# Kernel tuning notes

Measured on AMD Instinct MI355X. Metric: run time of the kernel, lower is better.

## Reference

```python
import jax, jax.numpy as jnp
import numpy as np

B, NA, C, NG = 32, 32768, 81, 24
POS_IOU, NEG_IOU, NPR = 0.5, 0.4, 3
VXY, VWH = 0.1, 0.2
NEG_BIG = 1e30


def cxcywh_to_xyxy(b):
    xy, wh = b[..., :2], b[..., 2:]
    return jnp.concatenate([xy - 0.5 * wh, xy + 0.5 * wh], axis=-1)


def box_iou_xyxy(a, g):
    # a: [Na,4], g: [Ng,4] -> [Na,Ng]
    lt = jnp.maximum(a[:, None, :2], g[None, :, :2])
    rb = jnp.minimum(a[:, None, 2:], g[None, :, 2:])
    wh = jnp.clip(rb - lt, 0.0)
    inter = wh[..., 0] * wh[..., 1]
    area_a = (a[:, 2] - a[:, 0]) * (a[:, 3] - a[:, 1])
    area_g = (g[:, 2] - g[:, 0]) * (g[:, 3] - g[:, 1])
    union = area_a[:, None] + area_g[None, :] - inter
    return inter / jnp.maximum(union, 1e-12)


def encode_ssd(gt, anc):
    # gt, anc: [N,4] cxcywh
    txy = (gt[:, :2] - anc[:, :2]) / anc[:, 2:] / VXY
    twh = jnp.log(gt[:, 2:] / anc[:, 2:]) / VWH
    return jnp.concatenate([txy, twh], axis=-1)


def match_one(anchors, gt_b, gt_l):
    # anchors: [Na,4], gt_b: [Ng,4], gt_l: [Ng]
    iou = box_iou_xyxy(cxcywh_to_xyxy(anchors), cxcywh_to_xyxy(gt_b))  # [Na,Ng]
    iou_max = iou.max(axis=1)
    gt_idx = jnp.argmax(iou, axis=1)          # [Na]
    best_anchor = jnp.argmax(iou, axis=0)     # [Ng]
    pos = (iou_max >= POS_IOU).at[best_anchor].set(True)
    ign = (iou_max > NEG_IOU) & ~pos
    cls_t = jnp.where(pos, gt_l[gt_idx].astype(jnp.int32), jnp.where(ign, -1, 0))
    box_t = encode_ssd(gt_b[gt_idx], anchors) * pos[:, None].astype(jnp.float32)
    return cls_t, box_t, pos


def setup_inputs() -> dict:
    key = jax.random.key(0)
    k1, k2, k3, k4, k5, k6, k7 = jax.random.split(key, 7)
    cls_pred = jax.random.normal(k1, (B, NA, C), jnp.float32)
    box_pred = jax.random.normal(k2, (B, NA, 4), jnp.float32) * 0.5
    a_xy = jax.random.uniform(k3, (NA, 2), jnp.float32)
    a_wh = jax.random.uniform(k4, (NA, 2), jnp.float32, minval=0.02, maxval=0.5)
    anchors = jnp.concatenate([a_xy, a_wh], axis=-1)
    g_xy = jax.random.uniform(k5, (B, NG, 2), jnp.float32)
    g_wh = jax.random.uniform(k6, (B, NG, 2), jnp.float32, minval=0.05, maxval=0.4)
    gt_boxes = jnp.concatenate([g_xy, g_wh], axis=-1)
    gt_labels = jax.random.randint(k7, (B, NG), 1, C, jnp.int32)
    return {"cls_pred": cls_pred, "box_pred": box_pred, "anchors": anchors,
            "gt_boxes": gt_boxes, "gt_labels": gt_labels}


def reference(cls_pred, box_pred, anchors, gt_boxes, gt_labels):
    # matching is @torch.no_grad -> constants
    cls_t, box_t, pos = jax.vmap(lambda b, l: match_one(anchors, b, l))(gt_boxes, gt_labels)
    box_t = jax.lax.stop_gradient(box_t)

    logp = jax.nn.log_softmax(cls_pred, axis=-1)
    tgt = jnp.clip(cls_t, 0)
    ce = -jnp.take_along_axis(logp, tgt[..., None], axis=-1)[..., 0]  # [B,Na]

    posf = pos.astype(jnp.float32)
    num_pos = posf.sum(-1)                       # [B]
    pos_ce_sum = (ce * posf).sum(-1)
    neg_mask = cls_t == 0
    neg_count = neg_mask.sum(-1).astype(jnp.float32)

    # descending sort of negative CE (hard-negative mining)
    neg_sorted = -jnp.sort(-jnp.where(neg_mask, ce, -NEG_BIG), axis=-1)  # [B,Na]
    ranks = jnp.arange(NA, dtype=jnp.float32)[None, :]

    num_neg = jnp.minimum(NPR * num_pos, neg_count)
    topk_sum = (neg_sorted * (ranks < num_neg[:, None])).sum(-1)
    cls_pos = jnp.where(num_neg > 0,
                        (pos_ce_sum + topk_sum) / jnp.maximum(num_pos + num_neg, 1.0),
                        pos_ce_sum / jnp.maximum(num_pos, 1.0))

    num_neg0 = jnp.minimum(100.0, neg_count)
    topk0_sum = (neg_sorted * (ranks < num_neg0[:, None])).sum(-1)
    cls_zero = jnp.where(num_neg0 > 0, topk0_sum / jnp.maximum(num_neg0, 1.0), 0.0)

    cls_loss = jnp.where(num_pos > 0, cls_pos, cls_zero)

    d = box_pred - box_t
    ad = jnp.abs(d)
    sl1 = jnp.where(ad < 1.0, 0.5 * d * d, ad - 0.5)
    reg_sum = (sl1 * posf[..., None]).sum((-1, -2))
    reg = jnp.where(num_pos > 0, reg_sum / jnp.maximum(num_pos * 4.0, 1.0), 0.0)

    return cls_loss.mean(), reg.mean(), num_pos.sum() / B
```

## Files before the change

### kernel.cpp

```cpp
#include <hip/hip_runtime.h>
#include <math.h>

#define B_  32
#define NA_ 32768
#define C_  81
#define NG_ 24

typedef const __attribute__((address_space(1))) unsigned int* gas_ptr;
typedef __attribute__((address_space(3))) unsigned int* las_ptr;

__device__ inline float wave_sum_f(float v) {
  #pragma unroll
  for (int s = 32; s >= 1; s >>= 1) v += __shfl_xor(v, s);
  return v;
}
__device__ inline int wave_sum_i(int v) {
  #pragma unroll
  for (int s = 32; s >= 1; s >>= 1) v += __shfl_xor(v, s);
  return v;
}
__device__ inline unsigned long long shflx_u64(unsigned long long v, int s) {
  int lo = __shfl_xor((int)(unsigned)(v & 0xFFFFFFFFULL), s);
  int hi = __shfl_xor((int)(unsigned)(v >> 32), s);
  return ((unsigned long long)(unsigned)hi << 32) | (unsigned)lo;
}

__global__ __launch_bounds__(256) void k_match_b(
    const float* __restrict__ anchors, const float* __restrict__ gt_boxes,
    int* __restrict__ best_anchor,
    int* num_pos_g, int* notneg_g, float* pos_ce_g, float* reg_sum_g, float* out)
{
  const int g = blockIdx.x, b = blockIdx.y;
  const int tid = threadIdx.x, wave = tid >> 6, lane = tid & 63;
  if (g == 0 && b == 0) {
    if (tid < B_) { num_pos_g[tid] = 0; notneg_g[tid] = 0; pos_ce_g[tid] = 0.f; reg_sum_g[tid] = 0.f; }
    else if (tid < B_ + 3) out[tid - B_] = 0.f;
  }
  const float* gp = gt_boxes + ((size_t)b * NG_ + g) * 4;
  const float gx0 = gp[0] - 0.5f * gp[2], gy0 = gp[1] - 0.5f * gp[3];
  const float gx1 = gp[0] + 0.5f * gp[2], gy1 = gp[1] + 0.5f * gp[3];
  const float area_g = (gx1 - gx0) * (gy1 - gy0);
  unsigned long long key = 0ULL;
  #pragma unroll 4
  for (int i = 0; i < NA_ / 256; ++i) {
    const int a = i * 256 + tid;
    const float4 anc = ((const float4*)anchors)[a];
    const float ax0 = anc.x - 0.5f * anc.z, ay0 = anc.y - 0.5f * anc.w;
    const float ax1 = anc.x + 0.5f * anc.z, ay1 = anc.y + 0.5f * anc.w;
    float lx = fmaxf(ax0, gx0), ly = fmaxf(ay0, gy0);
    float rx = fminf(ax1, gx1), ry = fminf(ay1, gy1);
    float ww = fmaxf(rx - lx, 0.f), hh = fmaxf(ry - ly, 0.f);
    float inter = ww * hh;
    float uni = (ax1 - ax0) * (ay1 - ay0) + area_g - inter;
    float iou = inter / fmaxf(uni, 1e-12f);
    unsigned long long k2 =
        ((unsigned long long)__float_as_uint(iou) << 32) | (unsigned)(~(unsigned)a);
    if (k2 > key) key = k2;
  }
  #pragma unroll
  for (int s = 32; s >= 1; s >>= 1) {
    unsigned long long o = shflx_u64(key, s);
    if (o > key) key = o;
  }
  __shared__ unsigned long long red[4];
  if (lane == 0) red[wave] = key;
  __syncthreads();
  if (tid == 0) {
    unsigned long long k = red[0];
    for (int w = 1; w < 4; ++w) if (red[w] > k) k = red[w];
    best_anchor[b * NG_ + g] = (int)(~(unsigned)k);
  }
}

#define NBLK 24
__device__ inline void stage_tile(const float* __restrict__ cls_pred,
                                  int b, int tile, las_ptr lbase, int tid)
{
  const unsigned int* gtile =
      (const unsigned int*)(cls_pred + ((size_t)b * NA_ + (size_t)tile * 64) * C_);
  #pragma unroll
  for (int k = 0; k < 20; ++k) {
    const int chunk = k * 64 + tid;
    __builtin_amdgcn_global_load_lds((gas_ptr)(gtile + (size_t)chunk * 4),
                                     lbase + (size_t)(k * 64) * 4, 16, 0, 0);
  }
  __builtin_amdgcn_global_load_lds((gas_ptr)(gtile + 5120 + tid),
                                   lbase + 5120, 4, 0, 0);
}

__global__ __launch_bounds__(64) void k_ce(
    const float* __restrict__ cls_pred, const float* __restrict__ box_pred,
    const float* __restrict__ anchors, const float* __restrict__ gt_boxes,
    const int* __restrict__ gt_labels, const int* __restrict__ best_anchor,
    int* __restrict__ neg_bits,
    int* __restrict__ num_pos_g, int* __restrict__ notneg_g,
    float* __restrict__ pos_ce_g, float* __restrict__ reg_sum_g)
{
  __shared__ float tile_sh[2][64 * C_];
  __shared__ float4 gt_xyxy[NG_];
  __shared__ float4 gt_cc[NG_];
  __shared__ float  gt_area[NG_];
  __shared__ int    label_sh[NG_];
  __shared__ int    best_a_sh[NG_];
  const int b = blockIdx.y;
  const int j = blockIdx.x;
  const int lane = threadIdx.x;

  if (lane < NG_) {
    const float* g = gt_boxes + ((size_t)b * NG_ + lane) * 4;
    const float cx = g[0], cy = g[1], w = g[2], h = g[3];
    const float x0 = cx - 0.5f * w, y0 = cy - 0.5f * h;
    const float x1 = cx + 0.5f * w, y1 = cy + 0.5f * h;
    gt_xyxy[lane] = make_float4(x0, y0, x1, y1);
    gt_cc[lane]   = make_float4(cx, cy, w, h);
    gt_area[lane] = (x1 - x0) * (y1 - y0);
    label_sh[lane]  = gt_labels[b * NG_ + lane];
    best_a_sh[lane] = best_anchor[b * NG_ + lane];
  }
  __syncthreads();

  const int p = lane & 3;
  const int wbase = (81 * lane) & ~3;

  int   npc = 0, nnc = 0;
  float pce = 0.f, regs = 0.f;

  int tj = j;
  stage_tile(cls_pred, b, tj, (las_ptr)tile_sh[0], lane);
  asm volatile("s_waitcnt vmcnt(0)" ::: "memory");
  __builtin_amdgcn_sched_barrier(0);
  int cur = 0;

  while (true) {
    const int tn = tj + NBLK;
    const bool more = (tn < NA_ / 64);
    if (more) stage_tile(cls_pred, b, tn, (las_ptr)tile_sh[cur ^ 1], lane);

    const int a = tj * 64 + lane;
    const size_t idx = (size_t)b * NA_ + a;

    const float4 anc = ((const float4*)anchors)[a];
    const float ax0 = anc.x - 0.5f * anc.z, ay0 = anc.y - 0.5f * anc.w;
    const float ax1 = anc.x + 0.5f * anc.z, ay1 = anc.y + 0.5f * anc.w;
    const float area_a = (ax1 - ax0) * (ay1 - ay0);
    float best_iou = -1.0f; int gi = 0;
    #pragma unroll 4
    for (int g = 0; g < NG_; ++g) {
      const float4 G = gt_xyxy[g];
      float lx = fmaxf(ax0, G.x), ly = fmaxf(ay0, G.y);
      float rx = fminf(ax1, G.z), ry = fminf(ay1, G.w);
      float ww = fmaxf(rx - lx, 0.f), hh = fmaxf(ry - ly, 0.f);
      float inter = ww * hh;
      float uni = area_a + gt_area[g] - inter;
      float iou = inter / fmaxf(uni, 1e-12f);
      if (iou > best_iou) { best_iou = iou; gi = g; }
    }
    bool pos = (best_iou >= 0.5f);
    #pragma unroll
    for (int g = 0; g < NG_; ++g) pos = pos || (best_a_sh[g] == a);
    const bool ign = (best_iou > 0.4f) && !pos;
    const bool neg = !pos && !ign;
    const int tgt = pos ? label_sh[gi] : 0;

    const float4* w4 = (const float4*)&tile_sh[cur][wbase];
    float s0 = 0.f, s1 = 0.f, s2 = 0.f, s3 = 0.f;
    #pragma unroll
    for (int k = 0; k < 21; ++k) {
      float4 v = w4[k];
      if (k == 0) {
        v.x = (p > 0) ? -1e30f : v.x;
        v.y = (p > 1) ? -1e30f : v.y;
        v.z = (p > 2) ? -1e30f : v.z;
      }
      if (k == 20) {
        v.y = (p < 1) ? -1e30f : v.y;
        v.z = (p < 2) ? -1e30f : v.z;
        v.w = (p < 3) ? -1e30f : v.w;
      }
      s0 += __expf(v.x); s1 += __expf(v.y);
      s2 += __expf(v.z); s3 += __expf(v.w);
    }
    const float sum = (s0 + s1) + (s2 + s3);
    const float tv = tile_sh[cur][81 * lane + tgt];
    const float ce = fmaxf(__logf(sum) - tv, 0.f);

    neg_bits[idx] = neg ? __float_as_int(ce) : -1;

    npc += pos;
    nnc += (pos || ign);
    if (pos) {
      pce += ce;
      const float4 bp = ((const float4*)box_pred)[idx];
      const float4 G  = gt_cc[gi];
      const float tx = (G.x - anc.x) / anc.z / 0.1f;
      const float ty = (G.y - anc.y) / anc.w / 0.1f;
      const float tw = logf(G.z / anc.z) / 0.2f;
      const float th = logf(G.w / anc.w) / 0.2f;
      float d, ad;
      d = bp.x - tx; ad = fabsf(d); regs += (ad < 1.f) ? 0.5f * d * d : (ad - 0.5f);
      d = bp.y - ty; ad = fabsf(d); regs += (ad < 1.f) ? 0.5f * d * d : (ad - 0.5f);
      d = bp.z - tw; ad = fabsf(d); regs += (ad < 1.f) ? 0.5f * d * d : (ad - 0.5f);
      d = bp.w - th; ad = fabsf(d); regs += (ad < 1.f) ? 0.5f * d * d : (ad - 0.5f);
    }

    if (!more) break;
    asm volatile("s_waitcnt vmcnt(0)" ::: "memory");
    __builtin_amdgcn_sched_barrier(0);
    tj = tn; cur ^= 1;
  }

  const int   np_w  = wave_sum_i(npc);
  const int   nn_w  = wave_sum_i(nnc);
  const float pce_w = wave_sum_f(pce);
  const float reg_w = wave_sum_f(regs);
  if (lane == 0) {
    if (np_w) atomicAdd(&num_pos_g[b], np_w);
    if (nn_w) atomicAdd(&notneg_g[b], nn_w);
    if (pce_w != 0.f) atomicAdd(&pos_ce_g[b], pce_w);
    if (reg_w != 0.f) atomicAdd(&reg_sum_g[b], reg_w);
  }
}

__global__ __launch_bounds__(1024) void k_select(
    const int* __restrict__ neg_bits,
    const int* __restrict__ num_pos_g, const int* __restrict__ notneg_g,
    const float* __restrict__ pos_ce_g, const float* __restrict__ reg_sum_g,
    float* __restrict__ out)
{
  const int b = blockIdx.x;
  const int t = threadIdx.x;
  const int wave = t >> 6, lane = t & 63;
  __shared__ unsigned cnt_sh[32];
  __shared__ float f1_sh[16], f0_sh[16];
  __shared__ unsigned cg_sh[16];
  if (t < 32) cnt_sh[t] = 0;
  int v[32];
  const int4* src4 = (const int4*)(neg_bits + (size_t)b * NA_);
  #pragma unroll
  for (int i = 0; i < 8; ++i) *(int4*)&v[4 * i] = src4[t + (i << 10)];
  const int np = num_pos_g[b];
  const int negc = NA_ - notneg_g[b];
  const int k1 = min(3 * np, negc);
  const int k0 = min(100, negc);
  __syncthreads();
  int T1 = 0, T0 = 0;
  for (int bit = 30; bit >= 0; --bit) {
    const int t1 = T1 | (1 << bit);
    const int t0 = T0 | (1 << bit);
    unsigned c = 0;
    #pragma unroll
    for (int i = 0; i < 32; ++i) {
      if (v[i] >= t1) c += (1u << 16);
      if (v[i] >= t0) c += 1u;
    }
    #pragma unroll
    for (int s = 32; s >= 1; s >>= 1) c += __shfl_xor(c, s);
    if (lane == 0) atomicAdd(&cnt_sh[bit], c);
    __syncthreads();
    const unsigned sum = cnt_sh[bit];
    if ((int)(sum >> 16) >= k1 && k1 > 0) T1 = t1;
    if ((int)(sum & 0xFFFFu) >= k0 && k0 > 0) T0 = t0;
  }
  float s1 = 0.f, s0 = 0.f; unsigned cg = 0;
  #pragma unroll
  for (int i = 0; i < 32; ++i) {
    const int x = v[i];
    if (x > T1) { s1 += __int_as_float(x); cg += (1u << 16); }
    if (x > T0) { s0 += __int_as_float(x); cg += 1u; }
  }
  #pragma unroll
  for (int s = 32; s >= 1; s >>= 1) {
    s1 += __shfl_xor(s1, s); s0 += __shfl_xor(s0, s); cg += __shfl_xor(cg, s);
  }
  if (lane == 0) { f1_sh[wave] = s1; f0_sh[wave] = s0; cg_sh[wave] = cg; }
  __syncthreads();
  if (t == 0) {
    float S1 = 0.f, S0 = 0.f; unsigned CG = 0;
    for (int w = 0; w < 16; ++w) { S1 += f1_sh[w]; S0 += f0_sh[w]; CG += cg_sh[w]; }
    const int cg1 = (int)(CG >> 16), cg0 = (int)(CG & 0xFFFFu);
    const float topk1 = (k1 > 0) ? (S1 + (float)(k1 - cg1) * __int_as_float(T1)) : 0.f;
    const float topk0 = (k0 > 0) ? (S0 + (float)(k0 - cg0) * __int_as_float(T0)) : 0.f;
    const float npf = (float)np;
    const float pce = pos_ce_g[b];
    float cls;
    if (np > 0)
      cls = (k1 > 0) ? (pce + topk1) / fmaxf(npf + (float)k1, 1.f)
                     : pce / fmaxf(npf, 1.f);
    else
      cls = (k0 > 0) ? topk0 / fmaxf((float)k0, 1.f) : 0.f;
    const float reg = (np > 0) ? reg_sum_g[b] / fmaxf(npf * 4.f, 1.f) : 0.f;
    atomicAdd(&out[0], cls * (1.0f / B_));
    atomicAdd(&out[1], reg * (1.0f / B_));
    atomicAdd(&out[2], npf * (1.0f / B_));
  }
}

extern "C" void kernel_launch(void* const* d_in, const int* in_sizes, int n_in,
                              void* d_out, int out_size, void* d_ws, size_t ws_size,
                              hipStream_t stream) {
  const float* cls_pred  = (const float*)d_in[0];
  const float* box_pred  = (const float*)d_in[1];
  const float* anchors   = (const float*)d_in[2];
  const float* gt_boxes  = (const float*)d_in[3];
  const int*   gt_labels = (const int*)d_in[4];
  float* out = (float*)d_out;

  char* ws = (char*)d_ws;
  int*   best_anchor = (int*)ws;
  int*   num_pos_g = (int*)(ws + 6144);
  int*   notneg_g  = (int*)(ws + 6144 + 128);
  float* pos_ce_g  = (float*)(ws + 6144 + 256);
  float* reg_sum_g = (float*)(ws + 6144 + 384);
  int*   neg_bits  = (int*)(ws + 8192);

  hipLaunchKernelGGL(k_match_b, dim3(NG_, B_), dim3(256), 0, stream,
                     anchors, gt_boxes, best_anchor,
                     num_pos_g, notneg_g, pos_ce_g, reg_sum_g, out);
  hipLaunchKernelGGL(k_ce, dim3(NBLK, B_), dim3(64), 0, stream,
                     cls_pred, box_pred, anchors, gt_boxes, gt_labels,
                     best_anchor, neg_bits,
                     num_pos_g, notneg_g, pos_ce_g, reg_sum_g);
  hipLaunchKernelGGL(k_select, dim3(B_), dim3(1024), 0, stream,
                     neg_bits, num_pos_g, notneg_g, pos_ce_g, reg_sum_g, out);
}
```

Before: 562.9 us.

## Stage CE tiles through registers with single LDS buffer and more blocks

Swaps the double-buffered direct global-to-LDS loads for prefetching the next class-score tile into 21 float4 registers. The registers are written to a single LDS buffer after the current tile has been consumed. Halving LDS use per block lets two blocks share a CU, and the grid per batch grows from 24 to 64 blocks to add parallelism. The cost is higher register pressure and an explicit LDS write pass.

```diff
diff --git a/kernel.cpp b/kernel.cpp
--- a/kernel.cpp
+++ b/kernel.cpp
@@ -5,9 +5,6 @@
 #define NA_ 32768
 #define C_  81
 #define NG_ 24
-
-typedef const __attribute__((address_space(1))) unsigned int* gas_ptr;
-typedef __attribute__((address_space(3))) unsigned int* las_ptr;
 
 __device__ inline float wave_sum_f(float v) {
   #pragma unroll
@@ -72,23 +69,8 @@
   }
 }
 
-#define NBLK 24
-__device__ inline void stage_tile(const float* __restrict__ cls_pred,
-                                  int b, int tile, las_ptr lbase, int tid)
-{
-  const unsigned int* gtile =
-      (const unsigned int*)(cls_pred + ((size_t)b * NA_ + (size_t)tile * 64) * C_);
-  #pragma unroll
-  for (int k = 0; k < 20; ++k) {
-    const int chunk = k * 64 + tid;
-    __builtin_amdgcn_global_load_lds((gas_ptr)(gtile + (size_t)chunk * 4),
-                                     lbase + (size_t)(k * 64) * 4, 16, 0, 0);
-  }
-  __builtin_amdgcn_global_load_lds((gas_ptr)(gtile + 5120 + tid),
-                                   lbase + 5120, 4, 0, 0);
-}
-
-__global__ __launch_bounds__(64) void k_ce(
+#define NBLK 64
+__global__ __launch_bounds__(64, 2) void k_ce(
     const float* __restrict__ cls_pred, const float* __restrict__ box_pred,
     const float* __restrict__ anchors, const float* __restrict__ gt_boxes,
     const int* __restrict__ gt_labels, const int* __restrict__ best_anchor,
@@ -96,7 +78,7 @@
     int* __restrict__ num_pos_g, int* __restrict__ notneg_g,
     float* __restrict__ pos_ce_g, float* __restrict__ reg_sum_g)
 {
-  __shared__ float tile_sh[2][64 * C_];
+  __shared__ float tile_sh[64 * C_];
   __shared__ float4 gt_xyxy[NG_];
   __shared__ float4 gt_cc[NG_];
   __shared__ float  gt_area[NG_];
@@ -125,16 +107,33 @@
   int   npc = 0, nnc = 0;
   float pce = 0.f, regs = 0.f;
 
+  float4 stg[20];
+  float4 stg_t;
+  const float4* bbase = (const float4*)(cls_pred + (size_t)b * NA_ * C_);
+
+  {
+    const float4* src = bbase + (size_t)j * (64 * C_ / 4);
+    #pragma unroll
+    for (int k = 0; k < 20; ++k) stg[k] = src[k * 64 + lane];
+    if (lane < 16) stg_t = src[1280 + lane];
+    float4* dst = (float4*)tile_sh;
+    #pragma unroll
+    for (int k = 0; k < 20; ++k) dst[k * 64 + lane] = stg[k];
+    if (lane < 16) dst[1280 + lane] = stg_t;
+  }
+
   int tj = j;
-  stage_tile(cls_pred, b, tj, (las_ptr)tile_sh[0], lane);
-  asm volatile("s_waitcnt vmcnt(0)" ::: "memory");
-  __builtin_amdgcn_sched_barrier(0);
-  int cur = 0;
-
-  while (true) {
-    const int tn = tj + NBLK;
-    const bool more = (tn < NA_ / 64);
-    if (more) stage_tile(cls_pred, b, tn, (las_ptr)tile_sh[cur ^ 1], lane);
+  #pragma unroll 1
+  for (int it = 0; it < NA_ / 64 / NBLK; ++it) {
+    const bool more = (it + 1 < NA_ / 64 / NBLK);
+
+    if (more) {
+      const float4* src = bbase + (size_t)(tj + NBLK) * (64 * C_ / 4);
+      #pragma unroll
+      for (int k = 0; k < 20; ++k) stg[k] = src[k * 64 + lane];
+      if (lane < 16) stg_t = src[1280 + lane];
+    }
+    __builtin_amdgcn_sched_barrier(0);
 
     const int a = tj * 64 + lane;
     const size_t idx = (size_t)b * NA_ + a;
@@ -162,7 +161,7 @@
     const bool neg = !pos && !ign;
     const int tgt = pos ? label_sh[gi] : 0;
 
-    const float4* w4 = (const float4*)&tile_sh[cur][wbase];
+    const float4* w4 = (const float4*)&tile_sh[wbase];
     float s0 = 0.f, s1 = 0.f, s2 = 0.f, s3 = 0.f;
     #pragma unroll
     for (int k = 0; k < 21; ++k) {
@@ -181,7 +180,7 @@
       s2 += __expf(v.z); s3 += __expf(v.w);
     }
     const float sum = (s0 + s1) + (s2 + s3);
-    const float tv = tile_sh[cur][81 * lane + tgt];
+    const float tv = tile_sh[81 * lane + tgt];
     const float ce = fmaxf(__logf(sum) - tv, 0.f);
 
     neg_bits[idx] = neg ? __float_as_int(ce) : -1;
@@ -203,10 +202,13 @@
       d = bp.w - th; ad = fabsf(d); regs += (ad < 1.f) ? 0.5f * d * d : (ad - 0.5f);
     }
 
-    if (!more) break;
-    asm volatile("s_waitcnt vmcnt(0)" ::: "memory");
-    __builtin_amdgcn_sched_barrier(0);
-    tj = tn; cur ^= 1;
+    if (more) {
+      float4* dst = (float4*)tile_sh;
+      #pragma unroll
+      for (int k = 0; k < 20; ++k) dst[k * 64 + lane] = stg[k];
+      if (lane < 16) dst[1280 + lane] = stg_t;
+    }
+    tj += NBLK;
   }
 
   const int   np_w  = wave_sum_i(npc);
```

New measurement: 637.4 us. 13.2% more time.
